# Kernel optimization log

Measured on AMD Instinct MI355X. Metric: run time of the kernel, lower is better.

Reference implementation:

```python
import jax, jax.numpy as jnp
import numpy as np

H = 16      # num_heads
DK = 128    # head_dim_qk
DV = 128    # head_dim_v
HID = 2048  # hidden_size
KS = 4      # conv kernel size


def _causal_dwconv(x, w, b):
    # x: [B, T, C], w: [C, KS], b: [C] -- depthwise causal conv (torch pads KS-1 then slices [:T])
    xc = jnp.transpose(x, (0, 2, 1))  # [B, C, T]
    out = jax.lax.conv_general_dilated(
        xc, w[:, None, :], window_strides=(1,), padding=[(KS - 1, 0)],
        feature_group_count=xc.shape[1], dimension_numbers=('NCH', 'OIH', 'NCH'))
    out = out + b[None, :, None]
    return jnp.transpose(out, (0, 2, 1))


def setup_inputs() -> dict:
    key = jax.random.key(0)
    ks = jax.random.split(key, 16)
    s = 0.02
    inp = {
        'x':   jax.random.normal(ks[0], (4, 2048, HID), jnp.float32),
        'Wq':  jax.random.normal(ks[1], (HID, H * DK), jnp.float32) * s,
        'Wk':  jax.random.normal(ks[2], (HID, H * DK), jnp.float32) * s,
        'Wv':  jax.random.normal(ks[3], (HID, H * DV), jnp.float32) * s,
        'Wa':  jax.random.normal(ks[4], (HID, H), jnp.float32) * s,
        'ba':  jnp.zeros((H,), jnp.float32),
        'Wb':  jax.random.normal(ks[5], (HID, H), jnp.float32) * s,
        'bb':  jnp.zeros((H,), jnp.float32),
        'Wg':  jax.random.normal(ks[6], (HID, H * DV), jnp.float32) * s,
        'Wo':  jax.random.normal(ks[7], (H * DV, HID), jnp.float32) * s,
        'qcw': jax.random.normal(ks[8], (H * DK, KS), jnp.float32) * 0.3,
        'qcb': jnp.zeros((H * DK,), jnp.float32),
        'kcw': jax.random.normal(ks[9], (H * DK, KS), jnp.float32) * 0.3,
        'kcb': jnp.zeros((H * DK,), jnp.float32),
        'vcw': jax.random.normal(ks[10], (H * DV, KS), jnp.float32) * 0.3,
        'vcb': jnp.zeros((H * DV,), jnp.float32),
        'ln_w': jnp.ones((DV,), jnp.float32),
        'ln_b': jnp.zeros((DV,), jnp.float32),
    }
    return inp


def _forward(x, Wq, Wk, Wv, Wa, ba, Wb, bb, Wg, Wo, qcw, qcb, kcw, kcb, vcw, vcb, ln_w, ln_b):
    B, T, _ = x.shape
    q = jax.nn.silu(_causal_dwconv(x @ Wq, qcw, qcb))
    k = jax.nn.silu(_causal_dwconv(x @ Wk, kcw, kcb))
    v = jax.nn.silu(_causal_dwconv(x @ Wv, vcw, vcb))
    q = q.reshape(B, T, H, DK)
    k = k.reshape(B, T, H, DK) * (DK ** -0.5)
    v = v.reshape(B, T, H, DV)
    alpha = jax.nn.sigmoid(x @ Wa + ba)  # [B, T, H]
    beta = jax.nn.sigmoid(x @ Wb + bb)   # [B, T, H]

    # time-major for scan
    qT = jnp.transpose(q, (1, 0, 2, 3))
    kT = jnp.transpose(k, (1, 0, 2, 3))
    vT = jnp.transpose(v, (1, 0, 2, 3))
    aT = jnp.transpose(alpha, (1, 0, 2))
    bT = jnp.transpose(beta, (1, 0, 2))

    def step(S, inps):
        qt, kt, vt, at, bt = inps
        Sk = jnp.einsum('bhvk,bhk->bhv', S, kt)            # S @ k
        err = Sk - vt
        S = at[..., None, None] * S - bt[..., None, None] * (err[..., None] * kt[:, :, None, :])
        ot = jnp.einsum('bhvk,bhk->bhv', S, qt)            # output uses NEW state
        return S, ot

    S0 = jnp.zeros((B, H, DV, DK), x.dtype)
    _, oT = jax.lax.scan(step, S0, (qT, kT, vT, aT, bT))    # [T, B, H, DV]
    o = jnp.transpose(oT, (1, 0, 2, 3))                      # [B, T, H, DV]

    # LayerNorm over head_dim_v (eps=1e-5)
    mu = jnp.mean(o, axis=-1, keepdims=True)
    var = jnp.mean(jnp.square(o - mu), axis=-1, keepdims=True)
    o = (o - mu) * jax.lax.rsqrt(var + 1e-5) * ln_w + ln_b

    g = jax.nn.sigmoid(x @ Wg).reshape(B, T, H, DV)
    o = (o * g).reshape(B, T, H * DV)
    return o @ Wo


def reference(x, Wq, Wk, Wv, Wa, ba, Wb, bb, Wg, Wo, qcw, qcb, kcw, kcb, vcw, vcb, ln_w, ln_b):
    return _forward(x, Wq, Wk, Wv, Wa, ba, Wb, bb, Wg, Wo, qcw, qcb, kcw, kcb, vcw, vcb, ln_w, ln_b)
```

## Files before the change

### kernel.cpp

```cpp
#include <hip/hip_runtime.h>
#include <stdint.h>

#define H_   16
#define DK_  128
#define DV_  128
#define HID_ 2048
#define KS_  4
#define B_   4
#define T_   2048
#define BT_  (B_*T_)
#define QKVC (3*HID_)
#define C_   32
#define RS_  32
#define NC_  (T_/C_)

typedef unsigned short u16;
typedef short  bf16x8 __attribute__((ext_vector_type(8)));
typedef u16    u16x8  __attribute__((ext_vector_type(8)));
typedef u16    u16x4  __attribute__((ext_vector_type(4)));
typedef float  f32x4  __attribute__((ext_vector_type(4)));

__device__ __forceinline__ float b2f(u16 u){
  union { unsigned int i; float f; } v; v.i = ((unsigned int)u) << 16; return v.f;
}
__device__ __forceinline__ u16 f2b(float f){
  unsigned int x = __float_as_uint(f);
  unsigned int r = (x + 0x7FFFu + ((x >> 16) & 1u)) >> 16;
  return (u16)r;
}
__device__ __forceinline__ float sigm(float x){ return 1.0f / (1.0f + __expf(-x)); }

#define MFMA16(a,b,c) __builtin_amdgcn_mfma_f32_16x16x32_bf16((a),(b),(c),0,0,0)

__global__ __launch_bounds__(256) void cvt_x_k(const f32x4* __restrict__ src,
                                               u16x4* __restrict__ dst, int n4)
{
  int i0 = blockIdx.x * 256 + threadIdx.x;
  int stride = gridDim.x * 256;
  for (int i = i0; i < n4; i += stride) {
    f32x4 v = src[i];
    u16x4 r; r[0] = f2b(v[0]); r[1] = f2b(v[1]); r[2] = f2b(v[2]); r[3] = f2b(v[3]);
    dst[i] = r;
  }
}

__global__ __launch_bounds__(256) void cvt_small_k(
    const float* __restrict__ qcw, const float* __restrict__ kcw, const float* __restrict__ vcw,
    const float* __restrict__ qcb, const float* __restrict__ kcb, const float* __restrict__ vcb,
    const float* __restrict__ ba,  const float* __restrict__ bb,
    const float* __restrict__ lnw, const float* __restrict__ lnb,
    u16* __restrict__ canon)
{
  int i = blockIdx.x * 256 + threadIdx.x;
  if (i >= 31008) return;
  float v;
  if (i < 24576) {
    const float* s = (i < 8192) ? qcw : (i < 16384) ? kcw : vcw;
    v = s[i & 8191];
  } else if (i < 30720) {
    int j = i - 24576;
    const float* s = (j < 2048) ? qcb : (j < 4096) ? kcb : vcb;
    v = s[j & 2047];
  } else if (i < 30752) {
    int j = i - 30720;
    v = (j < 16) ? ba[j] : bb[j - 16];
  } else {
    int j = i - 30752;
    v = (j < 128) ? lnw[j] : lnb[j - 128];
  }
  canon[i] = f2b(v);
}

__global__ __launch_bounds__(256) void transpose_b(const float* __restrict__ s0,
                                                   const float* __restrict__ s1,
                                                   const float* __restrict__ s2,
                                                   u16* __restrict__ dst,
                                                   int R, int C)
{
  int z = blockIdx.z;
  const float* src = (z == 0) ? s0 : (z == 1) ? s1 : s2;
  u16* d = dst + (size_t)z * R * C;
  __shared__ u16 t[32][33];
  int bx = blockIdx.x * 32;
  int by = blockIdx.y * 32;
  int lx = threadIdx.x & 31, ly = threadIdx.x >> 5;
  #pragma unroll
  for (int i = 0; i < 4; ++i) {
    int r = by + ly + i * 8, c = bx + lx;
    if (r < R && c < C) t[ly + i * 8][lx] = f2b(src[(size_t)r * C + c]);
  }
  __syncthreads();
  #pragma unroll
  for (int i = 0; i < 4; ++i) {
    int r = bx + ly + i * 8;
    int c = by + lx;
    if (r < C && c < R) d[(size_t)r * R + c] = t[lx][ly + i * 8];
  }
}

__device__ __forceinline__ void gload_lds16(const void* gp, void* lp){
  __builtin_amdgcn_global_load_lds(
      (const __attribute__((address_space(1))) void*)gp,
      (__attribute__((address_space(3))) void*)lp, 16, 0, 0);
}

#define GBM 256
#define GBN 256
#define GBK 64

__global__ __launch_bounds__(512, 2) void gemm256(const u16* __restrict__ A, int lda,
                                                  const u16* __restrict__ Bt, int ldb,
                                                  void* __restrict__ C, int ldc,
                                                  int K, int out_f32)
{
  __shared__ u16 lsA[2][GBM * GBK];
  __shared__ u16 lsB[2][GBN * GBK];
  int tid = threadIdx.x, wid = tid >> 6, lane = tid & 63;
  int l16 = lane & 15, quad = lane >> 4;
  int wr = wid >> 2, wc = wid & 3;

  int nbx = gridDim.x;
  int nwg = nbx * gridDim.y;
  int flat = blockIdx.y * nbx + blockIdx.x;
  int swzid = ((nwg & 7) == 0) ? ((flat & 7) * (nwg >> 3) + (flat >> 3)) : flat;
  int m0 = (swzid / nbx) * GBM;
  int n0 = (swzid % nbx) * GBN;

  f32x4 acc[8][4] = {};

  auto STAGE = [&](int t, int bi){
    int k0 = t * GBK;
    #pragma unroll
    for (int ld = 0; ld < 4; ++ld) {
      int slot = ld * 512 + tid;
      int row = slot >> 3, cg = slot & 7;
      int lofs = (ld * 512 + wid * 64) * 8;
      gload_lds16(A  + (size_t)(m0 + row) * lda + k0 + cg * 8, &lsA[bi][lofs]);
      gload_lds16(Bt + (size_t)(n0 + row) * ldb + k0 + cg * 8, &lsB[bi][lofs]);
    }
  };

  STAGE(0, 0);
  __syncthreads();

  int NT = K / GBK;
  for (int t = 0; t < NT; ++t) {
    int bi = t & 1;
    if (t + 1 < NT) STAGE(t + 1, bi ^ 1);
    const u16* pA = lsA[bi];
    const u16* pB = lsB[bi];
    #pragma unroll
    for (int ks = 0; ks < 2; ++ks) {
      bf16x8 bfr[4];
      #pragma unroll
      for (int ni = 0; ni < 4; ++ni)
        bfr[ni] = *(const bf16x8*)&pB[(wc * 64 + ni * 16 + l16) * GBK + ks * 32 + quad * 8];
      #pragma unroll
      for (int mi = 0; mi < 8; ++mi) {
        bf16x8 af = *(const bf16x8*)&pA[(wr * 128 + mi * 16 + l16) * GBK + ks * 32 + quad * 8];
        #pragma unroll
        for (int ni = 0; ni < 4; ++ni)
          acc[mi][ni] = MFMA16(af, bfr[ni], acc[mi][ni]);
      }
    }
    __syncthreads();
  }

  #pragma unroll
  for (int mi = 0; mi < 8; ++mi)
    #pragma unroll
    for (int ni = 0; ni < 4; ++ni)
      #pragma unroll
      for (int r = 0; r < 4; ++r) {
        int m = m0 + wr * 128 + mi * 16 + quad * 4 + r;
        int n = n0 + wc * 64 + ni * 16 + l16;
        if (out_f32) ((float*)C)[(size_t)m * ldc + n] = acc[mi][ni][r];
        else         ((u16*)C)[(size_t)m * ldc + n] = f2b(acc[mi][ni][r]);
      }
}

__global__ __launch_bounds__(256) void ab_k(const u16* __restrict__ x,
                                            const u16* __restrict__ WabT,
                                            const u16* __restrict__ ba,
                                            const u16* __restrict__ bb,
                                            float* __restrict__ ab)
{
  int j = threadIdx.x & 31, rl = threadIdx.x >> 5;
  int row = blockIdx.x * 8 + rl;
  const u16x8* xr = (const u16x8*)(x + (size_t)row * HID_);
  const u16x8* wr = (const u16x8*)(WabT + (size_t)j * HID_);
  float acc = 0.f;
  for (int k = 0; k < HID_ / 8; ++k) {
    u16x8 xv = xr[k], wv = wr[k];
    #pragma unroll
    for (int i = 0; i < 8; ++i) acc += b2f(xv[i]) * b2f(wv[i]);
  }
  float bias = (j < 16) ? b2f(ba[j]) : b2f(bb[j - 16]);
  float sg = sigm(acc + bias);
  if (j < 16) ab[(size_t)row * 16 + j] = sg;
  else        ab[(size_t)BT_ * 16 + (size_t)row * 16 + (j - 16)] = sg;
}

__global__ __launch_bounds__(256) void conv_silu_k(const u16* __restrict__ in,
                                                   const u16* __restrict__ cwv,
                                                   const u16* __restrict__ cbv,
                                                   u16* __restrict__ out)
{
  int idx  = blockIdx.x * 256 + threadIdx.x;
  int col8 = idx % (QKVC / 8);
  int t    = idx / (QKVC / 8);
  int col  = col8 * 8;
  int s = col >> 11;

  u16 wl[32];
  #pragma unroll
  for (int i = 0; i < 4; ++i)
    *(u16x8*)(wl + i * 8) = *(const u16x8*)(cwv + (size_t)col * KS_ + i * 8);
  u16x8 bv = *(const u16x8*)(cbv + col);

  float acc[8];
  #pragma unroll
  for (int j = 0; j < 8; ++j) acc[j] = b2f(bv[j]);

  #pragma unroll
  for (int tap = 0; tap < KS_; ++tap) {
    int tt = t - 3 + tap;
    if (tt >= 0) {
      u16x8 xv = *(const u16x8*)(in + (size_t)tt * QKVC + col);
      #pragma unroll
      for (int j = 0; j < 8; ++j) acc[j] = fmaf(b2f(xv[j]), b2f(wl[j * 4 + tap]), acc[j]);
    }
  }
  float scale = (s == 1) ? 0.08838834764831845f : 1.0f;
  u16x8 rv;
  #pragma unroll
  for (int j = 0; j < 8; ++j) {
    float a = acc[j];
    rv[j] = f2b(a * sigm(a) * scale);
  }
  *(u16x8*)(out + (size_t)t * QKVC + col) = rv;
}

__global__ __launch_bounds__(512) void chunk_scan_k(const u16* __restrict__ qkv,
                                                    const float* __restrict__ ab,
                                                    u16* __restrict__ o)
{
  __shared__ __align__(16) char smem[64896];
  u16 (*Kim)[136] = (u16(*)[136])(smem);
  u16 (*Qim)[136] = (u16(*)[136])(smem + 8704);
  u16 (*Sh)[136]  = (u16(*)[136])(smem + 17408);
  u16 (*Sl)[136]  = (u16(*)[136])(smem + 26112);
  u16 (*KT)[40]   = (u16(*)[40])(smem + 34816);
  u16 (*Vim)[32]  = (u16(*)[32])(smem + 45056);
  float (*KK)[36] = (float(*)[36])(smem + 47104);
  float (*KQ)[33] = (float(*)[33])(smem + 51712);
  float (*SK0)[33]= (float(*)[33])(smem + 55936);
  float (*SQ0)[33]= (float(*)[33])(smem + 60160);
  float (*PL4)[4] = (float(*)[4])(smem + 64384);
  float (*U)[33]  = (float(*)[33])(smem + 8704);

  int bid = blockIdx.x;
  int chain = bid & 63, rblk = bid >> 6;
  int b = chain >> 4, h = chain & 15;
  int tid = threadIdx.x, wv = tid >> 6, lane = tid & 63;
  int l16 = lane & 15, quad = lane >> 4;

  const u16* kbase = qkv + (size_t)b * T_ * QKVC + HID_ + h * DK_;
  const u16* qbase = qkv + (size_t)b * T_ * QKVC + h * DK_;
  const u16* vbase = qkv + (size_t)b * T_ * QKVC + 2 * HID_ + h * DV_ + rblk * RS_;
  const float* abase = ab + (size_t)b * T_ * 16 + h;
  const float* bbase = abase + (size_t)BT_ * 16;
  u16* obase = o + (size_t)b * T_ * 2048 + h * DV_ + rblk * RS_;

  f32x4 st[2];
  #pragma unroll
  for (int rt = 0; rt < 2; ++rt)
    #pragma unroll
    for (int r = 0; r < 4; ++r) st[rt][r] = 0.f;

  int jb = tid - 64;
  u16x8 stg[3];
  float avp = 0.f;

  auto LD = [&](int c) {
    int t0 = c * C_;
    if (wv == 0) {
      avp = (lane < 32) ? abase[(size_t)(t0 + lane) * 16]
                        : bbase[(size_t)(t0 + lane - 32) * 16];
    } else {
      #pragma unroll
      for (int it = 0; it < 3; ++it) {
        int j = jb + it * 448;
        if (j < 512) {
          int t = j >> 4, g = j & 15;
          stg[it] = *(const u16x8*)(kbase + (size_t)(t0 + t) * QKVC + g * 8);
        } else if (j < 1024) {
          int j2 = j - 512, t = j2 >> 4, g = j2 & 15;
          stg[it] = *(const u16x8*)(qbase + (size_t)(t0 + t) * QKVC + g * 8);
        } else if (j < 1152) {
          int j2 = j - 1024, t = j2 >> 2, rg = j2 & 3;
          stg[it] = *(const u16x8*)(vbase + (size_t)(t0 + t) * QKVC + rg * 8);
        }
      }
    }
  };

  LD(0);

  for (int c = 0; c < NC_; ++c) {
    int t0 = c * C_;

    #pragma unroll
    for (int rt = 0; rt < 2; ++rt)
      #pragma unroll
      for (int r = 0; r < 4; ++r) {
        float s = st[rt][r];
        u16 hi = f2b(s);
        float lo = s - b2f(hi);
        int row = rt * 16 + quad * 4 + r;
        int col = wv * 16 + l16;
        Sh[row][col] = hi;
        Sl[row][col] = f2b(lo);
      }

    if (wv == 0) {
      float av = avp;
      float p = av;
      #pragma unroll
      for (int d = 1; d < 32; d <<= 1) {
        float up = __shfl_up(p, d);
        if (lane >= d && lane < 32) p *= up;
      }
      float pm1 = __shfl_up(p, 1);
      float bt = __shfl(av, lane + 32);
      if (lane < 32) {
        if (lane == 0) pm1 = 1.f;
        f32x4 g;
        g[0] = bt * pm1; g[1] = bt; g[2] = 1.0f / p; g[3] = p;
        *(f32x4*)PL4[lane] = g;
      }
    } else {
      #pragma unroll
      for (int it = 0; it < 3; ++it) {
        int j = jb + it * 448;
        if (j < 512) {
          int t = j >> 4, g = j & 15;
          *(u16x8*)&Kim[t][g * 8] = stg[it];
          int blk = ((t >> 3) ^ (g & 3)) << 3;
          int tl = t & 7;
          #pragma unroll
          for (int e = 0; e < 8; ++e)
            KT[g * 8 + e][blk + tl] = stg[it][e];
        } else if (j < 1024) {
          int j2 = j - 512, t = j2 >> 4, g = j2 & 15;
          *(u16x8*)&Qim[t][g * 8] = stg[it];
        } else if (j < 1152) {
          int j2 = j - 1024, t = j2 >> 2, rg = j2 & 3;
          *(u16x8*)&Vim[t][rg * 8] = stg[it];
        }
      }
    }
    if (c + 1 < NC_) LD(c + 1);
    __syncthreads();

    {
      auto dotKK = [&](int mt, int nt) {
        f32x4 acc = {0.f,0.f,0.f,0.f};
        #pragma unroll
        for (int ks = 0; ks < 4; ++ks) {
          bf16x8 A = *(const bf16x8*)&Kim[mt * 16 + l16][ks * 32 + quad * 8];
          bf16x8 B = *(const bf16x8*)&Kim[nt * 16 + l16][ks * 32 + quad * 8];
          acc = MFMA16(A, B, acc);
        }
        #pragma unroll
        for (int r = 0; r < 4; ++r) KK[mt * 16 + quad * 4 + r][nt * 16 + l16] = acc[r];
      };
      auto dotKQ = [&](int mt, int nt) {
        f32x4 acc = {0.f,0.f,0.f,0.f};
        #pragma unroll
        for (int ks = 0; ks < 4; ++ks) {
          bf16x8 A = *(const bf16x8*)&Qim[mt * 16 + l16][ks * 32 + quad * 8];
          bf16x8 B = *(const bf16x8*)&Kim[nt * 16 + l16][ks * 32 + quad * 8];
          acc = MFMA16(A, B, acc);
        }
        #pragma unroll
        for (int r = 0; r < 4; ++r) KQ[mt * 16 + quad * 4 + r][nt * 16 + l16] = acc[r];
      };
      auto dotS = [&](const u16 (*Aarr)[136], int tt, int rr, float (*OUT)[33]) {
        f32x4 acc = {0.f,0.f,0.f,0.f};
        #pragma unroll
        for (int ks = 0; ks < 4; ++ks) {
          bf16x8 A  = *(const bf16x8*)&Aarr[tt * 16 + l16][ks * 32 + quad * 8];
          bf16x8 Bh = *(const bf16x8*)&Sh[rr * 16 + l16][ks * 32 + quad * 8];
          bf16x8 Bl = *(const bf16x8*)&Sl[rr * 16 + l16][ks * 32 + quad * 8];
          acc = MFMA16(A, Bh, acc);
          acc = MFMA16(A, Bl, acc);
        }
        #pragma unroll
        for (int r = 0; r < 4; ++r) OUT[tt * 16 + quad * 4 + r][rr * 16 + l16] = acc[r];
      };
      switch (wv) {
        case 0: dotS(Kim, 0, 0, SK0); dotKK(0, 0); break;
        case 1: dotS(Kim, 0, 1, SK0); dotKK(1, 0); break;
        case 2: dotS(Kim, 1, 0, SK0); dotKK(1, 1); break;
        case 3: dotS(Kim, 1, 1, SK0); dotKQ(0, 0); break;
        case 4: dotS(Qim, 0, 0, SQ0); dotKQ(1, 0); break;
        case 5: dotS(Qim, 0, 1, SQ0); dotKQ(1, 1); break;
        case 6: dotS(Qim, 1, 0, SQ0); break;
        default: dotS(Qim, 1, 1, SQ0); break;
      }
    }
    __syncthreads();

    union { u16x8 u; bf16x8 b; } gh, gl;
    int omt = (wv - 4) >> 1, ont = (wv - 4) & 1;
    if (wv == 0) {
      __builtin_amdgcn_s_setprio(1);
      if (lane < 32) {
        float ub[C_];
        #pragma unroll
        for (int t = 0; t < C_; ++t) {
          f32x4 g = *(const f32x4*)PL4[t];
          float u = g[0] * SK0[t][lane] - g[1] * b2f(Vim[t][lane]);
          float acc = 0.f;
          #pragma unroll
          for (int i4 = 0; i4 < t / 4; ++i4) {
            f32x4 kk = *(const f32x4*)&KK[t][i4 * 4];
            acc = fmaf(kk[0], ub[i4 * 4 + 0], acc);
            acc = fmaf(kk[1], ub[i4 * 4 + 1], acc);
            acc = fmaf(kk[2], ub[i4 * 4 + 2], acc);
            acc = fmaf(kk[3], ub[i4 * 4 + 3], acc);
          }
          #pragma unroll
          for (int i = (t / 4) * 4; i < t; ++i)
            acc = fmaf(KK[t][i], ub[i], acc);
          u = fmaf(-g[0], acc, u);
          U[t][lane] = u;
          ub[t] = g[2] * u;
        }
      }
      __builtin_amdgcn_s_setprio(0);
    } else if (wv >= 4) {
      int trow = omt * 16 + l16;
      float Pt = PL4[trow][3];
      #pragma unroll
      for (int e = 0; e < 8; ++e) {
        int i = quad * 8 + e;
        float gv = (i <= trow) ? (-Pt * PL4[i][2] * KQ[trow][i]) : 0.f;
        u16 h2 = f2b(gv);
        gh.u[e] = h2; gl.u[e] = f2b(gv - b2f(h2));
      }
    }
    __syncthreads();

    {
      float PL31 = PL4[31][3];

      #pragma unroll
      for (int rt = 0; rt < 2; ++rt) {
        union { u16x8 u; bf16x8 b; } ah, al;
        #pragma unroll
        for (int e = 0; e < 8; ++e) {
          int i = quad * 8 + e;
          float uv = U[i][rt * 16 + l16];
          float ucv = -PL31 * PL4[i][2] * uv;
          u16 hh = f2b(ucv);
          ah.u[e] = hh; al.u[e] = f2b(ucv - b2f(hh));
        }
        int col = wv * 16 + l16;
        bf16x8 Bk = *(const bf16x8*)&KT[col][(quad ^ ((col >> 3) & 3)) << 3];
        f32x4 cacc;
        #pragma unroll
        for (int r = 0; r < 4; ++r) cacc[r] = PL31 * st[rt][r];
        cacc = MFMA16(ah.b, Bk, cacc);
        cacc = MFMA16(al.b, Bk, cacc);
        st[rt] = cacc;
      }

      if (wv >= 4) {
        union { u16x8 u; bf16x8 b; } uth, utl;
        #pragma unroll
        for (int e = 0; e < 8; ++e) {
          int i = quad * 8 + e;
          float uv = U[i][ont * 16 + l16];
          u16 h1 = f2b(uv);
          uth.u[e] = h1; utl.u[e] = f2b(uv - b2f(h1));
        }
        f32x4 oacc;
        #pragma unroll
        for (int r = 0; r < 4; ++r) {
          int t = omt * 16 + quad * 4 + r;
          oacc[r] = PL4[t][3] * SQ0[t][ont * 16 + l16];
        }
        oacc = MFMA16(gh.b, uth.b, oacc);
        oacc = MFMA16(gh.b, utl.b, oacc);
        oacc = MFMA16(gl.b, uth.b, oacc);
        #pragma unroll
        for (int r = 0; r < 4; ++r) {
          int t = omt * 16 + quad * 4 + r;
          obase[(size_t)(t0 + t) * 2048 + ont * 16 + l16] = f2b(oacc[r]);
        }
      }
    }
    __syncthreads();
  }
}

__global__ __launch_bounds__(256) void ln_gate_k(const u16* __restrict__ o_raw,
                                                 const u16* __restrict__ g,
                                                 const u16* __restrict__ lnw,
                                                 const u16* __restrict__ lnb,
                                                 u16* __restrict__ o_ln)
{
  int gid = blockIdx.x * 4 + (threadIdx.x >> 6);
  int lane = threadIdx.x & 63;
  int row = gid >> 4, h = gid & 15;
  size_t ofs = (size_t)row * 2048 + h * 128 + lane * 2;
  unsigned int e2 = *(const unsigned int*)(o_raw + ofs);
  float ex = b2f((u16)(e2 & 0xffff)), ey = b2f((u16)(e2 >> 16));
  float s = ex + ey, ss = ex * ex + ey * ey;
  #pragma unroll
  for (int m = 1; m < 64; m <<= 1) { s += __shfl_xor(s, m); ss += __shfl_xor(ss, m); }
  float mean = s * (1.f / 128.f);
  float var  = ss * (1.f / 128.f) - mean * mean;
  float rstd = rsqrtf(fmaxf(var, 0.f) + 1e-5f);
  float w0 = b2f(lnw[lane * 2]), w1 = b2f(lnw[lane * 2 + 1]);
  float b0 = b2f(lnb[lane * 2]), b1 = b2f(lnb[lane * 2 + 1]);
  unsigned int g2 = *(const unsigned int*)(g + ofs);
  float g0 = sigm(b2f((u16)(g2 & 0xffff))), g1 = sigm(b2f((u16)(g2 >> 16)));
  float r0 = ((ex - mean) * rstd * w0 + b0) * g0;
  float r1 = ((ey - mean) * rstd * w1 + b1) * g1;
  *(unsigned int*)(o_ln + ofs) = (unsigned int)f2b(r0) | ((unsigned int)f2b(r1) << 16);
}

extern "C" void kernel_launch(void* const* d_in, const int* in_sizes, int n_in,
                              void* d_out, int out_size, void* d_ws, size_t ws_size,
                              hipStream_t stream)
{
  const float* x   = (const float*)d_in[0];
  const float* Wq  = (const float*)d_in[1];
  const float* Wk  = (const float*)d_in[2];
  const float* Wv  = (const float*)d_in[3];
  const float* Wa  = (const float*)d_in[4];
  const float* ba  = (const float*)d_in[5];
  const float* Wb  = (const float*)d_in[6];
  const float* bb  = (const float*)d_in[7];
  const float* Wg  = (const float*)d_in[8];
  const float* Wo  = (const float*)d_in[9];
  const float* qcw = (const float*)d_in[10];
  const float* qcb = (const float*)d_in[11];
  const float* kcw = (const float*)d_in[12];
  const float* kcb = (const float*)d_in[13];
  const float* vcw = (const float*)d_in[14];
  const float* vcb = (const float*)d_in[15];
  const float* lnw = (const float*)d_in[16];
  const float* lnb = (const float*)d_in[17];
  (void)in_sizes; (void)n_in; (void)out_size;

  char* ws = (char*)d_ws;
  size_t off = 0;
  auto alloc = [&](size_t bytes) -> void* {
    void* p = ws + off; off += (bytes + 255) & ~(size_t)255; return p;
  };
  u16* WT    = (u16*)alloc((size_t)3 * HID_ * HID_ * 2);
  u16* WabT  = (u16*)alloc((size_t)32 * HID_ * 2);
  u16* xc    = (u16*)alloc((size_t)BT_ * HID_ * 2);
  u16* canon = (u16*)alloc((size_t)31008 * 2);
  u16* post  = (u16*)alloc((size_t)BT_ * QKVC * 2);
  float* abuf = (float*)alloc((size_t)2 * BT_ * 16 * 4);
  size_t base_off = off;

  size_t fused_need = base_off + (((size_t)BT_ * QKVC * 2 + 255) & ~(size_t)255);
  int fused = (fused_need <= ws_size);
  u16* preC;
  if (fused) preC = (u16*)alloc((size_t)BT_ * QKVC * 2);
  else       preC = (u16*)alloc((size_t)BT_ * HID_ * 2 * 2);
  if (off > ws_size) return;

  u16* cw_c  = canon;
  u16* cb_c  = canon + 24576;
  u16* ba_c  = canon + 30720;
  u16* bb_c  = canon + 30736;
  u16* lnw_c = canon + 30752;
  u16* lnb_c = canon + 30880;

  u16* o_raw = preC;
  u16* g_raw = post;
  u16* o_ln  = post + (size_t)BT_ * HID_;
  u16* WTg   = WT;

  dim3 tb(256), tb5(512);

  cvt_x_k<<<dim3(4096), tb, 0, stream>>>((const f32x4*)x, (u16x4*)xc, BT_ * HID_ / 4);
  cvt_small_k<<<dim3(122), tb, 0, stream>>>(qcw, kcw, vcw, qcb, kcb, vcb, ba, bb, lnw, lnb, canon);

  transpose_b<<<dim3(64, 64, 3), tb, 0, stream>>>(Wq, Wk, Wv, WT, HID_, HID_);
  transpose_b<<<dim3(1, 64, 2), tb, 0, stream>>>(Wa, Wb, Wb, WabT, HID_, 16);

  if (fused) {
    gemm256<<<dim3(QKVC / GBN, BT_ / GBM), tb5, 0, stream>>>(xc, HID_, WT, HID_, preC, QKVC, HID_, 0);
    for (int b = 0; b < B_; ++b)
      conv_silu_k<<<dim3(T_ * (QKVC / 8) / 256), tb, 0, stream>>>(
          preC + (size_t)b * T_ * QKVC, cw_c, cb_c, post + (size_t)b * T_ * QKVC);
  } else {
    for (int b = 0; b < B_; ++b) {
      const u16* xb = xc + (size_t)b * T_ * HID_;
      gemm256<<<dim3(QKVC / GBN, T_ / GBM), tb5, 0, stream>>>(xb, HID_, WT, HID_, preC, QKVC, HID_, 0);
      conv_silu_k<<<dim3(T_ * (QKVC / 8) / 256), tb, 0, stream>>>(
          preC, cw_c, cb_c, post + (size_t)b * T_ * QKVC);
    }
  }

  transpose_b<<<dim3(64, 64, 2), tb, 0, stream>>>(Wg, Wo, Wo, WTg, HID_, HID_);

  ab_k<<<dim3(BT_ / 8), tb, 0, stream>>>(xc, WabT, ba_c, bb_c, abuf);

  chunk_scan_k<<<dim3(256), tb5, 0, stream>>>(post, abuf, o_raw);

  gemm256<<<dim3(HID_ / GBN, BT_ / GBM), tb5, 0, stream>>>(xc, HID_, WTg, HID_, g_raw, HID_, HID_, 0);

  ln_gate_k<<<dim3(BT_ * H_ / 4), tb, 0, stream>>>(o_raw, g_raw, lnw_c, lnb_c, o_ln);

  gemm256<<<dim3(HID_ / GBN, BT_ / GBM), tb5, 0, stream>>>(o_ln, HID_,
      WT + (size_t)HID_ * HID_, HID_, d_out, HID_, HID_, 1);
}
```

Before: 1.236 ms.

## Double-buffer chunk inputs and precompute next chunk's KK/KQ during serial solve

Double-buffers the K, Q, K-transpose, V, KK and KQ shared-memory tiles, with global loads issued two chunks ahead. The state-independent KK and KQ Gram products for the next chunk now run on waves 1-6 while wave 0 does the serial triangular solve. This takes that work off the critical path between barriers. In exchange, shared memory grows to about 105 KB per block, which may lower occupancy, and staging registers stay live longer.

```diff
diff --git a/kernel.cpp b/kernel.cpp
--- a/kernel.cpp
+++ b/kernel.cpp
@@ -245,19 +245,13 @@
                                                     const float* __restrict__ ab,
                                                     u16* __restrict__ o)
 {
-  __shared__ __align__(16) char smem[64896];
-  u16 (*Kim)[136] = (u16(*)[136])(smem);
-  u16 (*Qim)[136] = (u16(*)[136])(smem + 8704);
-  u16 (*Sh)[136]  = (u16(*)[136])(smem + 17408);
-  u16 (*Sl)[136]  = (u16(*)[136])(smem + 26112);
-  u16 (*KT)[40]   = (u16(*)[40])(smem + 34816);
-  u16 (*Vim)[32]  = (u16(*)[32])(smem + 45056);
-  float (*KK)[36] = (float(*)[36])(smem + 47104);
-  float (*KQ)[33] = (float(*)[33])(smem + 51712);
-  float (*SK0)[33]= (float(*)[33])(smem + 55936);
-  float (*SQ0)[33]= (float(*)[33])(smem + 60160);
-  float (*PL4)[4] = (float(*)[4])(smem + 64384);
-  float (*U)[33]  = (float(*)[33])(smem + 8704);
+  __shared__ __align__(16) char smem[107648];
+  float (*SK0)[33] = (float(*)[33])(smem + 94464);
+  float (*SQ0)[33] = (float(*)[33])(smem + 98688);
+  float (*PL4)[4]  = (float(*)[4])(smem + 102912);
+  float (*U)[33]   = (float(*)[33])(smem + 103424);
+  u16 (*Sh)[136]   = (u16(*)[136])(smem + 34816);
+  u16 (*Sl)[136]   = (u16(*)[136])(smem + 43520);
 
   int bid = blockIdx.x;
   int chain = bid & 63, rblk = bid >> 6;
@@ -282,33 +276,120 @@
   u16x8 stg[3];
   float avp = 0.f;
 
-  auto LD = [&](int c) {
+  auto LDA = [&](int c) {
     int t0 = c * C_;
-    if (wv == 0) {
-      avp = (lane < 32) ? abase[(size_t)(t0 + lane) * 16]
-                        : bbase[(size_t)(t0 + lane - 32) * 16];
-    } else {
-      #pragma unroll
-      for (int it = 0; it < 3; ++it) {
-        int j = jb + it * 448;
-        if (j < 512) {
-          int t = j >> 4, g = j & 15;
-          stg[it] = *(const u16x8*)(kbase + (size_t)(t0 + t) * QKVC + g * 8);
-        } else if (j < 1024) {
-          int j2 = j - 512, t = j2 >> 4, g = j2 & 15;
-          stg[it] = *(const u16x8*)(qbase + (size_t)(t0 + t) * QKVC + g * 8);
-        } else if (j < 1152) {
-          int j2 = j - 1024, t = j2 >> 2, rg = j2 & 3;
-          stg[it] = *(const u16x8*)(vbase + (size_t)(t0 + t) * QKVC + rg * 8);
-        }
-      }
-    }
-  };
-
-  LD(0);
+    avp = (lane < 32) ? abase[(size_t)(t0 + lane) * 16]
+                      : bbase[(size_t)(t0 + lane - 32) * 16];
+  };
+  auto LDI = [&](int c) {
+    int t0 = c * C_;
+    #pragma unroll
+    for (int it = 0; it < 3; ++it) {
+      int j = jb + it * 448;
+      if (j < 512) {
+        int t = j >> 4, g = j & 15;
+        stg[it] = *(const u16x8*)(kbase + (size_t)(t0 + t) * QKVC + g * 8);
+      } else if (j < 1024) {
+        int j2 = j - 512, t = j2 >> 4, g = j2 & 15;
+        stg[it] = *(const u16x8*)(qbase + (size_t)(t0 + t) * QKVC + g * 8);
+      } else if (j < 1152) {
+        int j2 = j - 1024, t = j2 >> 2, rg = j2 & 3;
+        stg[it] = *(const u16x8*)(vbase + (size_t)(t0 + t) * QKVC + rg * 8);
+      }
+    }
+  };
+  auto WIM = [&](int p) {
+    u16 (*Kim)[136] = (u16(*)[136])(smem + p * 8704);
+    u16 (*Qim)[136] = (u16(*)[136])(smem + 17408 + p * 8704);
+    u16 (*KT)[40]   = (u16(*)[40])(smem + 52224 + p * 10240);
+    u16 (*Vim)[32]  = (u16(*)[32])(smem + 72704 + p * 2048);
+    #pragma unroll
+    for (int it = 0; it < 3; ++it) {
+      int j = jb + it * 448;
+      if (j < 512) {
+        int t = j >> 4, g = j & 15;
+        *(u16x8*)&Kim[t][g * 8] = stg[it];
+        int blk = ((t >> 3) ^ (g & 3)) << 3;
+        int tl = t & 7;
+        #pragma unroll
+        for (int e = 0; e < 8; ++e)
+          KT[g * 8 + e][blk + tl] = stg[it][e];
+      } else if (j < 1024) {
+        int j2 = j - 512, t = j2 >> 4, g = j2 & 15;
+        *(u16x8*)&Qim[t][g * 8] = stg[it];
+      } else if (j < 1152) {
+        int j2 = j - 1024, t = j2 >> 2, rg = j2 & 3;
+        *(u16x8*)&Vim[t][rg * 8] = stg[it];
+      }
+    }
+  };
+  auto dotKK = [&](const u16 (*Kim)[136], float (*KK)[36], int mt, int nt) {
+    f32x4 acc = {0.f,0.f,0.f,0.f};
+    #pragma unroll
+    for (int ks = 0; ks < 4; ++ks) {
+      bf16x8 A = *(const bf16x8*)&Kim[mt * 16 + l16][ks * 32 + quad * 8];
+      bf16x8 B = *(const bf16x8*)&Kim[nt * 16 + l16][ks * 32 + quad * 8];
+      acc = MFMA16(A, B, acc);
+    }
+    #pragma unroll
+    for (int r = 0; r < 4; ++r) KK[mt * 16 + quad * 4 + r][nt * 16 + l16] = acc[r];
+  };
+  auto dotKQ = [&](const u16 (*Qim)[136], const u16 (*Kim)[136], float (*KQ)[33],
+                   int mt, int nt) {
+    f32x4 acc = {0.f,0.f,0.f,0.f};
+    #pragma unroll
+    for (int ks = 0; ks < 4; ++ks) {
+      bf16x8 A = *(const bf16x8*)&Qim[mt * 16 + l16][ks * 32 + quad * 8];
+      bf16x8 B = *(const bf16x8*)&Kim[nt * 16 + l16][ks * 32 + quad * 8];
+      acc = MFMA16(A, B, acc);
+    }
+    #pragma unroll
+    for (int r = 0; r < 4; ++r) KQ[mt * 16 + quad * 4 + r][nt * 16 + l16] = acc[r];
+  };
+  auto dotS = [&](const u16 (*Aarr)[136], int tt, int rr, float (*OUT)[33]) {
+    f32x4 acc = {0.f,0.f,0.f,0.f};
+    #pragma unroll
+    for (int ks = 0; ks < 4; ++ks) {
+      bf16x8 A  = *(const bf16x8*)&Aarr[tt * 16 + l16][ks * 32 + quad * 8];
+      bf16x8 Bh = *(const bf16x8*)&Sh[rr * 16 + l16][ks * 32 + quad * 8];
+      bf16x8 Bl = *(const bf16x8*)&Sl[rr * 16 + l16][ks * 32 + quad * 8];
+      acc = MFMA16(A, Bh, acc);
+      acc = MFMA16(A, Bl, acc);
+    }
+    #pragma unroll
+    for (int r = 0; r < 4; ++r) OUT[tt * 16 + quad * 4 + r][rr * 16 + l16] = acc[r];
+  };
+
+  if (wv == 0) LDA(0);
+  else { LDI(0); WIM(0); LDI(1); }
+  __syncthreads();
+  {
+    const u16 (*Kim0)[136] = (const u16(*)[136])(smem);
+    const u16 (*Qim0)[136] = (const u16(*)[136])(smem + 17408);
+    float (*KK0)[36] = (float(*)[36])(smem + 76800);
+    float (*KQ0)[33] = (float(*)[33])(smem + 86016);
+    if (wv >= 1 && wv <= 3) {
+      const int mts[3] = {0, 1, 1}, nts[3] = {0, 0, 1};
+      dotKK(Kim0, KK0, mts[wv - 1], nts[wv - 1]);
+    } else if (wv >= 4 && wv <= 6) {
+      const int mts[3] = {0, 1, 1}, nts[3] = {0, 0, 1};
+      dotKQ(Qim0, Kim0, KQ0, mts[wv - 4], nts[wv - 4]);
+    }
+  }
 
   for (int c = 0; c < NC_; ++c) {
     int t0 = c * C_;
+    int pc = c & 1, pn = pc ^ 1;
+    const u16 (*KimC)[136] = (const u16(*)[136])(smem + pc * 8704);
+    const u16 (*QimC)[136] = (const u16(*)[136])(smem + 17408 + pc * 8704);
+    const u16 (*KTC)[40]   = (const u16(*)[40])(smem + 52224 + pc * 10240);
+    const u16 (*VimC)[32]  = (const u16(*)[32])(smem + 72704 + pc * 2048);
+    const float (*KKC)[36] = (const float(*)[36])(smem + 76800 + pc * 4608);
+    const float (*KQC)[33] = (const float(*)[33])(smem + 86016 + pc * 4224);
+    const u16 (*KimN)[136] = (const u16(*)[136])(smem + pn * 8704);
+    const u16 (*QimN)[136] = (const u16(*)[136])(smem + 17408 + pn * 8704);
+    float (*KKN)[36] = (float(*)[36])(smem + 76800 + pn * 4608);
+    float (*KQN)[33] = (float(*)[33])(smem + 86016 + pn * 4224);
 
     #pragma unroll
     for (int rt = 0; rt < 2; ++rt)
@@ -339,77 +420,15 @@
         g[0] = bt * pm1; g[1] = bt; g[2] = 1.0f / p; g[3] = p;
         *(f32x4*)PL4[lane] = g;
       }
+      if (c + 1 < NC_) LDA(c + 1);
     } else {
-      #pragma unroll
-      for (int it = 0; it < 3; ++it) {
-        int j = jb + it * 448;
-        if (j < 512) {
-          int t = j >> 4, g = j & 15;
-          *(u16x8*)&Kim[t][g * 8] = stg[it];
-          int blk = ((t >> 3) ^ (g & 3)) << 3;
-          int tl = t & 7;
-          #pragma unroll
-          for (int e = 0; e < 8; ++e)
-            KT[g * 8 + e][blk + tl] = stg[it][e];
-        } else if (j < 1024) {
-          int j2 = j - 512, t = j2 >> 4, g = j2 & 15;
-          *(u16x8*)&Qim[t][g * 8] = stg[it];
-        } else if (j < 1152) {
-          int j2 = j - 1024, t = j2 >> 2, rg = j2 & 3;
-          *(u16x8*)&Vim[t][rg * 8] = stg[it];
-        }
-      }
-    }
-    if (c + 1 < NC_) LD(c + 1);
+      if (c + 1 < NC_) WIM(pn);
+      if (c + 2 < NC_) LDI(c + 2);
+    }
     __syncthreads();
 
-    {
-      auto dotKK = [&](int mt, int nt) {
-        f32x4 acc = {0.f,0.f,0.f,0.f};
-        #pragma unroll
-        for (int ks = 0; ks < 4; ++ks) {
-          bf16x8 A = *(const bf16x8*)&Kim[mt * 16 + l16][ks * 32 + quad * 8];
-          bf16x8 B = *(const bf16x8*)&Kim[nt * 16 + l16][ks * 32 + quad * 8];
-          acc = MFMA16(A, B, acc);
-        }
-        #pragma unroll
-        for (int r = 0; r < 4; ++r) KK[mt * 16 + quad * 4 + r][nt * 16 + l16] = acc[r];
-      };
-      auto dotKQ = [&](int mt, int nt) {
-        f32x4 acc = {0.f,0.f,0.f,0.f};
-        #pragma unroll
-        for (int ks = 0; ks < 4; ++ks) {
-          bf16x8 A = *(const bf16x8*)&Qim[mt * 16 + l16][ks * 32 + quad * 8];
-          bf16x8 B = *(const bf16x8*)&Kim[nt * 16 + l16][ks * 32 + quad * 8];
-          acc = MFMA16(A, B, acc);
-        }
-        #pragma unroll
-        for (int r = 0; r < 4; ++r) KQ[mt * 16 + quad * 4 + r][nt * 16 + l16] = acc[r];
-      };
-      auto dotS = [&](const u16 (*Aarr)[136], int tt, int rr, float (*OUT)[33]) {
-        f32x4 acc = {0.f,0.f,0.f,0.f};
-        #pragma unroll
-        for (int ks = 0; ks < 4; ++ks) {
-          bf16x8 A  = *(const bf16x8*)&Aarr[tt * 16 + l16][ks * 32 + quad * 8];
-          bf16x8 Bh = *(const bf16x8*)&Sh[rr * 16 + l16][ks * 32 + quad * 8];
-          bf16x8 Bl = *(const bf16x8*)&Sl[rr * 16 + l16][ks * 32 + quad * 8];
-          acc = MFMA16(A, Bh, acc);
-          acc = MFMA16(A, Bl, acc);
-        }
-        #pragma unroll
-        for (int r = 0; r < 4; ++r) OUT[tt * 16 + quad * 4 + r][rr * 16 + l16] = acc[r];
-      };
-      switch (wv) {
-        case 0: dotS(Kim, 0, 0, SK0); dotKK(0, 0); break;
-        case 1: dotS(Kim, 0, 1, SK0); dotKK(1, 0); break;
-        case 2: dotS(Kim, 1, 0, SK0); dotKK(1, 1); break;
-        case 3: dotS(Kim, 1, 1, SK0); dotKQ(0, 0); break;
-        case 4: dotS(Qim, 0, 0, SQ0); dotKQ(1, 0); break;
-        case 5: dotS(Qim, 0, 1, SQ0); dotKQ(1, 1); break;
-        case 6: dotS(Qim, 1, 0, SQ0); break;
-        default: dotS(Qim, 1, 1, SQ0); break;
-      }
-    }
+    if (wv < 4) dotS(KimC, wv >> 1, wv & 1, SK0);
+    else        dotS(QimC, (wv - 4) >> 1, (wv - 4) & 1, SQ0);
     __syncthreads();
 
     union { u16x8 u; bf16x8 b; } gh, gl;
@@ -421,11 +440,11 @@
         #pragma unroll
         for (int t = 0; t < C_; ++t) {
           f32x4 g = *(const f32x4*)PL4[t];
-          float u = g[0] * SK0[t][lane] - g[1] * b2f(Vim[t][lane]);
+          float u = g[0] * SK0[t][lane] - g[1] * b2f(VimC[t][lane]);
           float acc = 0.f;
           #pragma unroll
           for (int i4 = 0; i4 < t / 4; ++i4) {
-            f32x4 kk = *(const f32x4*)&KK[t][i4 * 4];
+            f32x4 kk = *(const f32x4*)&KKC[t][i4 * 4];
             acc = fmaf(kk[0], ub[i4 * 4 + 0], acc);
             acc = fmaf(kk[1], ub[i4 * 4 + 1], acc);
             acc = fmaf(kk[2], ub[i4 * 4 + 2], acc);
@@ -433,20 +452,29 @@
           }
           #pragma unroll
           for (int i = (t / 4) * 4; i < t; ++i)
-            acc = fmaf(KK[t][i], ub[i], acc);
+            acc = fmaf(KKC[t][i], ub[i], acc);
           u = fmaf(-g[0], acc, u);
           U[t][lane] = u;
           ub[t] = g[2] * u;
         }
       }
       __builtin_amdgcn_s_setprio(0);
-    } else if (wv >= 4) {
+    } else if (wv <= 3) {
+      if (c + 1 < NC_) {
+        const int mts[3] = {0, 1, 1}, nts[3] = {0, 0, 1};
+        dotKK(KimN, KKN, mts[wv - 1], nts[wv - 1]);
+      }
+    } else {
+      if (wv <= 6 && c + 1 < NC_) {
+        const int mts[3] = {0, 1, 1}, nts[3] = {0, 0, 1};
+        dotKQ(QimN, KimN, KQN, mts[wv - 4], nts[wv - 4]);
+      }
       int trow = omt * 16 + l16;
       float Pt = PL4[trow][3];
       #pragma unroll
       for (int e = 0; e < 8; ++e) {
         int i = quad * 8 + e;
-        float gv = (i <= trow) ? (-Pt * PL4[i][2] * KQ[trow][i]) : 0.f;
+        float gv = (i <= trow) ? (-Pt * PL4[i][2] * KQC[trow][i]) : 0.f;
         u16 h2 = f2b(gv);
         gh.u[e] = h2; gl.u[e] = f2b(gv - b2f(h2));
       }
@@ -468,7 +496,7 @@
           ah.u[e] = hh; al.u[e] = f2b(ucv - b2f(hh));
         }
         int col = wv * 16 + l16;
-        bf16x8 Bk = *(const bf16x8*)&KT[col][(quad ^ ((col >> 3) & 3)) << 3];
+        bf16x8 Bk = *(const bf16x8*)&KTC[col][(quad ^ ((col >> 3) & 3)) << 3];
         f32x4 cacc;
         #pragma unroll
         for (int r = 0; r < 4; ++r) cacc[r] = PL31 * st[rt][r];
```

Result: no change. 1.221 ms (-1.2%).
